# Optimization experiments

Measured on AMD Instinct MI355X. Metric: run time of the kernel, lower is better.

## Reference

```python
import jax, jax.numpy as jnp
import numpy as np

C = 1.0          # curvature
MIN_NORM = 1e-15
EPS = 1e-7       # atanh clamp for fp32

def _sqnorm(x):
    return jnp.sum(x * x, axis=-1, keepdims=True)

def _norm(x):
    return jnp.sqrt(jnp.maximum(_sqnorm(x), MIN_NORM))

def _atanh(u):
    return jnp.arctanh(jnp.clip(u, -1.0 + EPS, 1.0 - EPS))

def mobius_add(x, y, c):
    x2 = _sqnorm(x); y2 = _sqnorm(y)
    xy = jnp.sum(x * y, axis=-1, keepdims=True)
    num = (1.0 + 2.0 * c * xy + c * y2) * x + (1.0 - c * x2) * y
    den = 1.0 + 2.0 * c * xy + c * c * x2 * y2
    return num / jnp.maximum(den, MIN_NORM)

def logmap0(p, c):
    sc = jnp.sqrt(c)
    pn = _norm(p)
    return p / pn / sc * _atanh(sc * pn)

def logmap(p1, p2, c):
    # tangent vector at p1 pointing to p2 (Poincare ball)
    sub = mobius_add(-p1, p2, c)
    sn = _norm(sub)
    lam = 2.0 / jnp.maximum(1.0 - c * _sqnorm(p1), MIN_NORM)
    sc = jnp.sqrt(c)
    return 2.0 / sc / lam * _atanh(sc * sn) * sub / sn

def expmap(p, u, c):
    un = _norm(u)
    lam = 2.0 / jnp.maximum(1.0 - c * _sqnorm(p), MIN_NORM)
    sc = jnp.sqrt(c)
    second = jnp.tanh(sc * lam * un / 2.0) * u / (sc * un)
    return mobius_add(p, second, c)


def setup_inputs() -> dict:
    key = jax.random.key(0)
    k1, k2, k3 = jax.random.split(key, 3)
    B, N, D = 1, 1024, 128
    # points inside the unit Poincare ball (||x|| ~ 0.23)
    x = jax.random.normal(k1, (B, N, D), jnp.float32) * 0.02
    # sparse-ish dense adjacency mask (0/1 floats)
    adj = (jax.random.uniform(k2, (B, N, N)) < 0.05).astype(jnp.float32)
    # DenseAtt: nn.Linear(2*D, 1) weight (flattened) + bias
    att_w = jax.random.normal(k3, (2 * D,), jnp.float32) * 0.1
    att_b = jnp.zeros((), jnp.float32)
    return {"x": x, "adj": adj, "att_w": att_w, "att_b": att_b}


def reference(x, adj, att_w, att_b):
    B, N, D = x.shape
    x_t = logmap0(x, C)                                   # [B,N,D]
    # DenseAtt: sigmoid(Linear(cat(x_i, x_j))) decomposed as left_i + right_j + b
    left = x_t @ att_w[:D]                                # [B,N]
    right = x_t @ att_w[D:]                               # [B,N]
    att = jax.nn.sigmoid(left[:, :, None] + right[:, None, :] + att_b) * adj  # [B,N,N]
    # pairwise logmap: tangent at x_i of every x_j  -> [B,N,N,D]
    x_local = logmap(x[:, :, None, :], x[:, None, :, :], C)
    support_t = jnp.einsum('bij,bijd->bid', att, x_local)  # [B,N,D]
    return expmap(x, support_t, C)
```

## Files before the change

kernel.cpp:

```cpp
#include <hip/hip_runtime.h>
#include <math.h>


typedef short short4v __attribute__((ext_vector_type(4)));
typedef short short8v __attribute__((ext_vector_type(8)));
typedef float float4v __attribute__((ext_vector_type(4)));

static __device__ __forceinline__ short f2bf(float f) {
    unsigned u = __float_as_uint(f);
    u += 0x7fff + ((u >> 16) & 1);
    return (short)(u >> 16);
}
static __device__ __forceinline__ float rcpf(float x) { return __builtin_amdgcn_rcpf(x); }
static __device__ __forceinline__ short8v ld8(const unsigned short* p) {
    short4v lo = *(const short4v*)p;
    short4v hi = *(const short4v*)(p + 4);
    return (short8v){lo[0],lo[1],lo[2],lo[3],hi[0],hi[1],hi[2],hi[3]};
}
static __device__ __forceinline__ float dot4(float4v a, float4v b) {
    return a[0]*b[0] + a[1]*b[1] + a[2]*b[2] + a[3]*b[3];
}
static __device__ __forceinline__ float atanh_over(float pn) {
    float uu = fminf(pn, 1.f - 1e-7f);
    return 0.5f * __logf((1.f + uu) * rcpf(1.f - uu)) * rcpf(pn);
}

__global__ __launch_bounds__(256) void hyp_stats(
    const float* __restrict__ x, const float* __restrict__ w,
    const float* __restrict__ battp,
    float* __restrict__ st_x2, float* __restrict__ st_L, float* __restrict__ st_R)
{
    int row  = blockIdx.x * 4 + (threadIdx.x >> 6);
    int lane = threadIdx.x & 63;
    const float* xr = x + row * 128;
    float a0 = xr[lane], a1 = xr[lane + 64];
    float x2 = a0 * a0 + a1 * a1;
    float dl = a0 * w[lane]       + a1 * w[lane + 64];
    float dr = a0 * w[lane + 128] + a1 * w[lane + 192];
    for (int m = 1; m < 64; m <<= 1) {
        x2 += __shfl_xor(x2, m);
        dl += __shfl_xor(dl, m);
        dr += __shfl_xor(dr, m);
    }
    if (lane == 0) {
        float pn = sqrtf(fmaxf(x2, 1e-15f));
        float f  = atanh_over(pn);
        st_x2[row] = x2;
        st_L[row]  = f * dl + battp[0];
        st_R[row]  = f * dr;
    }
}

__global__ __launch_bounds__(256, 2) void hyp_main(
    const float* __restrict__ x, const float* __restrict__ adj,
    const float* __restrict__ st_x2, const float* __restrict__ st_L,
    const float* __restrict__ st_R,
    float* __restrict__ Yp, float* __restrict__ Sp2)
{
    __shared__ unsigned short sXI [16 * 132];
    __shared__ unsigned short sXJ [128 * 132];
    __shared__ unsigned short sXJt[128 * 132];
    __shared__ unsigned short sW  [16 * 132];

    const int t    = threadIdx.x;
    const int lane = t & 63;
    const int wave = t >> 6;
    const int n    = lane & 15;
    const int q    = lane >> 4;
    const int i0   = blockIdx.x * 16;
    const int c    = blockIdx.y;
    const int j0   = c * 128;

    const float4v* x4 = (const float4v*)x;

    float x2i4[4], bi4[4], li4[4];
#pragma unroll
    for (int r = 0; r < 4; ++r) {
        int i = i0 + q * 4 + r;
        x2i4[r] = st_x2[i];
        li4[r]  = st_L[i];
    }
    float x2j2[2], rj2[2], adjv[2][4];
#pragma unroll
    for (int jsl = 0; jsl < 2; ++jsl) {
        int j = j0 + (wave * 2 + jsl) * 16 + n;
        x2j2[jsl] = st_x2[j];
        rj2[jsl]  = st_R[j];
#pragma unroll
        for (int r = 0; r < 4; ++r)
            adjv[jsl][r] = adj[(i0 + q * 4 + r) * 1024 + j];
    }
#pragma unroll
    for (int r = 0; r < 4; ++r) bi4[r] = 1.f - x2i4[r];

#pragma unroll
    for (int it = 0; it < 2; ++it) {
        int idx = t + it * 256;
        int r = idx >> 5, cc = idx & 31;
        float4v v = x4[(i0 + r) * 32 + cc];
        short4v h = { f2bf(v[0]), f2bf(v[1]), f2bf(v[2]), f2bf(v[3]) };
        *(short4v*)&sXI[r * 132 + cc * 4] = h;
    }
#pragma unroll
    for (int it = 0; it < 4; ++it) {
        int bid = t + it * 256;
        int jr = ((bid >> 4) & 3) | (((bid >> 6) & 7) << 2);
        int dc = (bid & 15) | (((bid >> 9) & 1) << 4);
        float4v v[4];
#pragma unroll
        for (int e = 0; e < 4; ++e)
            v[e] = x4[(j0 + jr * 4 + e) * 32 + dc];
        short4v h[4];
#pragma unroll
        for (int e = 0; e < 4; ++e) {
            h[e] = (short4v){ f2bf(v[e][0]), f2bf(v[e][1]), f2bf(v[e][2]), f2bf(v[e][3]) };
            *(short4v*)&sXJ[(jr * 4 + e) * 132 + dc * 4] = h[e];
        }
#pragma unroll
        for (int d = 0; d < 4; ++d) {
            short4v ht = (short4v){ h[0][d], h[1][d], h[2][d], h[3][d] };
            *(short4v*)&sXJt[(dc * 4 + d) * 132 + jr * 4] = ht;
        }
    }
    __syncthreads();

    short8v afrag[4];
#pragma unroll
    for (int kk = 0; kk < 4; ++kk)
        afrag[kk] = ld8(&sXI[n * 132 + kk * 32 + q * 8]);

    float Sacc[4] = {0.f, 0.f, 0.f, 0.f};

#pragma unroll
    for (int jsl = 0; jsl < 2; ++jsl) {
        int js = wave * 2 + jsl;
        int jrow = js * 16 + n;
        float4v acc = (float4v){0.f, 0.f, 0.f, 0.f};
#pragma unroll
        for (int kk = 0; kk < 4; ++kk) {
            short8v b = ld8(&sXJ[jrow * 132 + kk * 32 + q * 8]);
            acc = __builtin_amdgcn_mfma_f32_16x16x32_bf16(afrag[kk], b, acc, 0, 0, 0);
        }
        float x2j = x2j2[jsl];
        float rj  = rj2[jsl];
#pragma unroll
        for (int r = 0; r < 4; ++r) {
            float G     = acc[r];
            int   i     = q * 4 + r;
            float alpha = 1.f - 2.f * G + x2j;
            float den   = fmaxf(fmaf(x2i4[r], x2j, 1.f - 2.f * G), 1e-15f);
            float rdn   = rcpf(den);
            float bb    = bi4[r];
            float nn2   = alpha * alpha * x2i4[r] + bb * bb * x2j - 2.f * alpha * bb * G;
            float sn    = sqrtf(fmaxf(nn2 * rdn * rdn, 1e-15f));
            float tt    = atanh_over(sn);
            float z     = li4[r] + rj;
            float sig   = rcpf(1.f + __expf(-z));
            float g     = sig * adjv[jsl][r] * tt * rdn;
            Sacc[r]     = fmaf(g, alpha, Sacc[r]);
            sW[i * 132 + js * 16 + n] = (unsigned short)f2bf(g);
        }
    }
    __syncthreads();

    float4v accB[2];
    accB[0] = (float4v){0.f, 0.f, 0.f, 0.f};
    accB[1] = (float4v){0.f, 0.f, 0.f, 0.f};
#pragma unroll
    for (int nsl = 0; nsl < 2; ++nsl) {
        int ns = wave * 2 + nsl;
#pragma unroll
        for (int kk = 0; kk < 4; ++kk) {
            short8v a = ld8(&sW  [n * 132 + kk * 32 + q * 8]);
            short8v b = ld8(&sXJt[(ns * 16 + n) * 132 + kk * 32 + q * 8]);
            accB[nsl] = __builtin_amdgcn_mfma_f32_16x16x32_bf16(a, b, accB[nsl], 0, 0, 0);
        }
    }

    float* Yc = Yp + c * 131072;
#pragma unroll
    for (int nsl = 0; nsl < 2; ++nsl) {
        int ns = wave * 2 + nsl;
#pragma unroll
        for (int r = 0; r < 4; ++r)
            Yc[(i0 + q * 4 + r) * 128 + ns * 16 + n] = accB[nsl][r];
    }
#pragma unroll
    for (int r = 0; r < 4; ++r)
        Sp2[((c * 1024 + i0 + q * 4 + r) * 4 + wave) * 16 + n] = Sacc[r];
}

__global__ __launch_bounds__(256) void hyp_exp(
    const float* __restrict__ x, const float* __restrict__ Yp,
    const float* __restrict__ Sp2, const float* __restrict__ st_x2,
    float* __restrict__ out)
{
    const int t   = threadIdx.x;
    const int row = blockIdx.x * 8 + (t >> 5);
    const int l32 = t & 31;
    float4v y = (float4v){0.f, 0.f, 0.f, 0.f};
    float S = 0.f;
#pragma unroll
    for (int c = 0; c < 8; ++c) {
        y += *(const float4v*)&Yp[c * 131072 + row * 128 + l32 * 4];
        S += Sp2[(c * 1024 + row) * 64 + l32];
        S += Sp2[(c * 1024 + row) * 64 + 32 + l32];
    }
#pragma unroll
    for (int m = 1; m < 32; m <<= 1) S += __shfl_xor(S, m, 32);

    float4v xa = ((const float4v*)x)[row * 32 + l32];
    float x2 = st_x2[row];
    float bE = fmaxf(1.f - x2, 1e-15f);
    float u[4], un2p = 0.f, xup = 0.f;
#pragma unroll
    for (int e = 0; e < 4; ++e) {
        u[e] = bE * (bE * y[e] - S * xa[e]);
        un2p += u[e] * u[e];
        xup  += xa[e] * u[e];
    }
#pragma unroll
    for (int m = 1; m < 32; m <<= 1) {
        un2p += __shfl_xor(un2p, m, 32);
        xup  += __shfl_xor(xup,  m, 32);
    }
    float un  = sqrtf(fmaxf(un2p, 1e-15f));
    float e2  = __expf(2.f * un * rcpf(bE));
    float th  = 1.f - 2.f * rcpf(e2 + 1.f);
    float s2  = th * rcpf(un);
    float xy  = s2 * xup;
    float y2s = th * th;
    float coef = 1.f + 2.f * xy + y2s;
    float den  = fmaxf(1.f + 2.f * xy + x2 * y2s, 1e-15f);
    float rd   = rcpf(den);
    float4v o = { (coef*xa[0] + bE*s2*u[0])*rd, (coef*xa[1] + bE*s2*u[1])*rd,
                  (coef*xa[2] + bE*s2*u[2])*rd, (coef*xa[3] + bE*s2*u[3])*rd };
    ((float4v*)out)[row * 32 + l32] = o;
}

extern "C" void kernel_launch(void* const* d_in, const int* in_sizes, int n_in,
                              void* d_out, int out_size, void* d_ws, size_t ws_size,
                              hipStream_t stream) {
    const float* x    = (const float*)d_in[0];
    const float* adj  = (const float*)d_in[1];
    const float* w    = (const float*)d_in[2];
    const float* batt = (const float*)d_in[3];
    float* out = (float*)d_out;

    float* Yp    = (float*)d_ws;
    float* Sp2   = Yp + 8 * 131072;
    float* st_x2 = Sp2 + 8 * 1024 * 64;
    float* st_L  = st_x2 + 1024;
    float* st_R  = st_L + 1024;

    hipLaunchKernelGGL(hyp_stats, dim3(256), dim3(256), 0, stream,
                       x, w, batt, st_x2, st_L, st_R);
    hipLaunchKernelGGL(hyp_main, dim3(64, 8), dim3(256), 0, stream,
                       x, adj, st_x2, st_L, st_R, Yp, Sp2);
    hipLaunchKernelGGL(hyp_exp, dim3(128), dim3(256), 0, stream,
                       x, Yp, Sp2, st_x2, out);
}
```

Baseline: 72.27 us.

## Precompute swizzled bf16 X and transpose in prep kernel, load via global_load_lds

The stats kernel becomes a prep kernel that also converts x to bf16 in an XOR-swizzled layout and writes a transposed swizzled copy to workspace. The main kernel then fills its LDS tiles with direct global-to-LDS 16-byte loads instead of converting and transposing fp32 data in every block. Shared tiles drop the padding and use XOR swizzling to avoid bank conflicts while allowing 16-byte LDS reads. The trade-off is that the prep kernel runs on only 16 blocks with serial per-thread work, and each block does a full-vmcnt wait before the barrier.

```diff
diff --git a/kernel.cpp b/kernel.cpp
--- a/kernel.cpp
+++ b/kernel.cpp
@@ -11,12 +11,10 @@
     u += 0x7fff + ((u >> 16) & 1);
     return (short)(u >> 16);
 }
+static __device__ __forceinline__ float bf2f(unsigned short s) {
+    return __uint_as_float(((unsigned)s) << 16);
+}
 static __device__ __forceinline__ float rcpf(float x) { return __builtin_amdgcn_rcpf(x); }
-static __device__ __forceinline__ short8v ld8(const unsigned short* p) {
-    short4v lo = *(const short4v*)p;
-    short4v hi = *(const short4v*)(p + 4);
-    return (short8v){lo[0],lo[1],lo[2],lo[3],hi[0],hi[1],hi[2],hi[3]};
-}
 static __device__ __forceinline__ float dot4(float4v a, float4v b) {
     return a[0]*b[0] + a[1]*b[1] + a[2]*b[2] + a[3]*b[3];
 }
@@ -24,43 +22,101 @@
     float uu = fminf(pn, 1.f - 1e-7f);
     return 0.5f * __logf((1.f + uu) * rcpf(1.f - uu)) * rcpf(pn);
 }
-
-__global__ __launch_bounds__(256) void hyp_stats(
+static __device__ __forceinline__ void glds16(const void* g, void* l) {
+    __builtin_amdgcn_global_load_lds(
+        (const __attribute__((address_space(1))) void*)g,
+        (__attribute__((address_space(3))) void*)l, 16, 0, 0);
+}
+
+__global__ __launch_bounds__(256) void hyp_prep(
     const float* __restrict__ x, const float* __restrict__ w,
     const float* __restrict__ battp,
+    unsigned short* __restrict__ XbSw, unsigned short* __restrict__ XbtSw,
     float* __restrict__ st_x2, float* __restrict__ st_L, float* __restrict__ st_R)
 {
-    int row  = blockIdx.x * 4 + (threadIdx.x >> 6);
-    int lane = threadIdx.x & 63;
-    const float* xr = x + row * 128;
-    float a0 = xr[lane], a1 = xr[lane + 64];
-    float x2 = a0 * a0 + a1 * a1;
-    float dl = a0 * w[lane]       + a1 * w[lane + 64];
-    float dr = a0 * w[lane + 128] + a1 * w[lane + 192];
-    for (int m = 1; m < 64; m <<= 1) {
-        x2 += __shfl_xor(x2, m);
-        dl += __shfl_xor(dl, m);
-        dr += __shfl_xor(dr, m);
-    }
-    if (lane == 0) {
-        float pn = sqrtf(fmaxf(x2, 1e-15f));
-        float f  = atanh_over(pn);
-        st_x2[row] = x2;
-        st_L[row]  = f * dl + battp[0];
-        st_R[row]  = f * dr;
+    __shared__ __align__(16) unsigned short sT[128 * 128];
+    __shared__ float sWf[256];
+    __shared__ float sPx[256], sPl[256], sPr[256];
+    const int t  = threadIdx.x;
+    const int bx = blockIdx.x;
+    const bool typeA = bx < 8;
+    const int c  = typeA ? bx : bx - 8;
+    const float4v* x4 = (const float4v*)x;
+    const float4v* w4 = (const float4v*)w;
+
+    if (t < 64) *(float4v*)&sWf[t * 4] = w4[t];
+
+#pragma unroll
+    for (int it = 0; it < 16; ++it) {
+        int idx  = t + it * 256;
+        int r    = idx >> 5;
+        int col4 = idx & 31;
+        float4v v = x4[(c * 128 + r) * 32 + col4];
+        short4v h = { f2bf(v[0]), f2bf(v[1]), f2bf(v[2]), f2bf(v[3]) };
+        int pos = (col4 >> 1) ^ (r & 15);
+        int off = r * 128 + pos * 8 + (col4 & 1) * 4;
+        *(short4v*)&sT[off] = h;
+        if (typeA) *(short4v*)&XbSw[c * 16384 + off] = h;
+    }
+    __syncthreads();
+
+    if (typeA) {
+        int j = t >> 1, ph = t & 1;
+        float x2 = 0.f, dl = 0.f, dr = 0.f;
+#pragma unroll
+        for (int p = 0; p < 8; ++p) {
+            int pp = ph * 8 + p;
+            short8v v = *(const short8v*)&sT[j * 128 + pp * 8];
+            int kbase = (pp ^ (j & 15)) * 8;
+#pragma unroll
+            for (int e = 0; e < 8; ++e) {
+                float f = bf2f((unsigned short)v[e]);
+                x2 = fmaf(f, f, x2);
+                dl = fmaf(f, sWf[kbase + e], dl);
+                dr = fmaf(f, sWf[128 + kbase + e], dr);
+            }
+        }
+        sPx[t] = x2; sPl[t] = dl; sPr[t] = dr;
+        __syncthreads();
+        if (t < 128) {
+            float x2s = sPx[2 * t] + sPx[2 * t + 1];
+            float dls = sPl[2 * t] + sPl[2 * t + 1];
+            float drs = sPr[2 * t] + sPr[2 * t + 1];
+            float pn  = sqrtf(fmaxf(x2s, 1e-15f));
+            float f   = atanh_over(pn);
+            int row = c * 128 + t;
+            st_x2[row] = x2s;
+            st_L [row] = dls * f + battp[0];
+            st_R [row] = drs * f;
+        }
+    } else {
+        int d = t >> 1, jh = t & 1;
+        unsigned short tmp[64];
+#pragma unroll
+        for (int jj = 0; jj < 64; ++jj) {
+            int j = jh * 64 + jj;
+            tmp[jj] = sT[j * 128 + (((d >> 3) ^ (j & 15)) * 8) + (d & 7)];
+        }
+#pragma unroll
+        for (int k8 = 0; k8 < 8; ++k8) {
+            int ktl = jh * 8 + k8;
+            int pt  = ktl ^ (d & 15);
+            *(short8v*)&XbtSw[c * 16384 + d * 128 + pt * 8] = *(const short8v*)&tmp[k8 * 8];
+        }
     }
 }
 
 __global__ __launch_bounds__(256, 2) void hyp_main(
-    const float* __restrict__ x, const float* __restrict__ adj,
+    const unsigned short* __restrict__ XbSw, const unsigned short* __restrict__ XbtSw,
+    const float* __restrict__ adj,
     const float* __restrict__ st_x2, const float* __restrict__ st_L,
     const float* __restrict__ st_R,
     float* __restrict__ Yp, float* __restrict__ Sp2)
 {
-    __shared__ unsigned short sXI [16 * 132];
-    __shared__ unsigned short sXJ [128 * 132];
-    __shared__ unsigned short sXJt[128 * 132];
-    __shared__ unsigned short sW  [16 * 132];
+    __shared__ __align__(16) unsigned short sXI [16 * 128];
+    __shared__ __align__(16) unsigned short sXJ [128 * 128];
+    __shared__ __align__(16) unsigned short sXJt[128 * 128];
+    __shared__ __align__(16) unsigned short sW  [16 * 128];
 
     const int t    = threadIdx.x;
     const int lane = t & 63;
@@ -71,8 +127,6 @@
     const int c    = blockIdx.y;
     const int j0   = c * 128;
 
-    const float4v* x4 = (const float4v*)x;
-
     float x2i4[4], bi4[4], li4[4];
 #pragma unroll
     for (int r = 0; r < 4; ++r) {
@@ -93,43 +147,27 @@
 #pragma unroll
     for (int r = 0; r < 4; ++r) bi4[r] = 1.f - x2i4[r];
 
-#pragma unroll
-    for (int it = 0; it < 2; ++it) {
-        int idx = t + it * 256;
-        int r = idx >> 5, cc = idx & 31;
-        float4v v = x4[(i0 + r) * 32 + cc];
-        short4v h = { f2bf(v[0]), f2bf(v[1]), f2bf(v[2]), f2bf(v[3]) };
-        *(short4v*)&sXI[r * 132 + cc * 4] = h;
-    }
-#pragma unroll
-    for (int it = 0; it < 4; ++it) {
-        int bid = t + it * 256;
-        int jr = ((bid >> 4) & 3) | (((bid >> 6) & 7) << 2);
-        int dc = (bid & 15) | (((bid >> 9) & 1) << 4);
-        float4v v[4];
-#pragma unroll
-        for (int e = 0; e < 4; ++e)
-            v[e] = x4[(j0 + jr * 4 + e) * 32 + dc];
-        short4v h[4];
-#pragma unroll
-        for (int e = 0; e < 4; ++e) {
-            h[e] = (short4v){ f2bf(v[e][0]), f2bf(v[e][1]), f2bf(v[e][2]), f2bf(v[e][3]) };
-            *(short4v*)&sXJ[(jr * 4 + e) * 132 + dc * 4] = h[e];
-        }
-#pragma unroll
-        for (int d = 0; d < 4; ++d) {
-            short4v ht = (short4v){ h[0][d], h[1][d], h[2][d], h[3][d] };
-            *(short4v*)&sXJt[(dc * 4 + d) * 132 + jr * 4] = ht;
-        }
-    }
+    {
+        const char* gXI  = (const char*)(XbSw + i0 * 128);
+        const char* gXJ  = (const char*)(XbSw + c * 16384);
+        const char* gXJt = (const char*)(XbtSw + c * 16384);
+        int wo = wave * 1024 + lane * 16;
+        glds16(gXI + wo, (char*)sXI + wo);
+#pragma unroll
+        for (int it = 0; it < 8; ++it) {
+            glds16(gXJ  + it * 4096 + wo, (char*)sXJ  + it * 4096 + wo);
+            glds16(gXJt + it * 4096 + wo, (char*)sXJt + it * 4096 + wo);
+        }
+    }
+    __builtin_amdgcn_s_waitcnt(0);
     __syncthreads();
 
     short8v afrag[4];
 #pragma unroll
     for (int kk = 0; kk < 4; ++kk)
-        afrag[kk] = ld8(&sXI[n * 132 + kk * 32 + q * 8]);
-
-    float Sacc[4] = {0.f, 0.f, 0.f, 0.f};
+        afrag[kk] = *(const short8v*)&sXI[n * 128 + (((kk * 4 + q) ^ n)) * 8];
+
+    float Sacc[4];
 
 #pragma unroll
     for (int jsl = 0; jsl < 2; ++jsl) {
@@ -138,7 +176,7 @@
         float4v acc = (float4v){0.f, 0.f, 0.f, 0.f};
 #pragma unroll
         for (int kk = 0; kk < 4; ++kk) {
-            short8v b = ld8(&sXJ[jrow * 132 + kk * 32 + q * 8]);
+            short8v b = *(const short8v*)&sXJ[jrow * 128 + (((kk * 4 + q) ^ n)) * 8];
             acc = __builtin_amdgcn_mfma_f32_16x16x32_bf16(afrag[kk], b, acc, 0, 0, 0);
         }
         float x2j = x2j2[jsl];
@@ -157,8 +195,8 @@
             float z     = li4[r] + rj;
             float sig   = rcpf(1.f + __expf(-z));
             float g     = sig * adjv[jsl][r] * tt * rdn;
-            Sacc[r]     = fmaf(g, alpha, Sacc[r]);
-            sW[i * 132 + js * 16 + n] = (unsigned short)f2bf(g);
+            if (jsl == 0) Sacc[r] = g * alpha; else Sacc[r] = fmaf(g, alpha, Sacc[r]);
+            sW[i * 128 + ((js * 2 + (n >> 3)) ^ i) * 8 + (n & 7)] = (unsigned short)f2bf(g);
         }
     }
     __syncthreads();
@@ -169,10 +207,11 @@
 #pragma unroll
     for (int nsl = 0; nsl < 2; ++nsl) {
         int ns = wave * 2 + nsl;
+        int drow = ns * 16 + n;
 #pragma unroll
         for (int kk = 0; kk < 4; ++kk) {
-            short8v a = ld8(&sW  [n * 132 + kk * 32 + q * 8]);
-            short8v b = ld8(&sXJt[(ns * 16 + n) * 132 + kk * 32 + q * 8]);
+            short8v a = *(const short8v*)&sW  [n * 128    + (((kk * 4 + q) ^ n)) * 8];
+            short8v b = *(const short8v*)&sXJt[drow * 128 + (((kk * 4 + q) ^ n)) * 8];
             accB[nsl] = __builtin_amdgcn_mfma_f32_16x16x32_bf16(a, b, accB[nsl], 0, 0, 0);
         }
     }
@@ -252,11 +291,13 @@
     float* st_x2 = Sp2 + 8 * 1024 * 64;
     float* st_L  = st_x2 + 1024;
     float* st_R  = st_L + 1024;
-
-    hipLaunchKernelGGL(hyp_stats, dim3(256), dim3(256), 0, stream,
-                       x, w, batt, st_x2, st_L, st_R);
+    unsigned short* XbSw  = (unsigned short*)(st_R + 1024);
+    unsigned short* XbtSw = XbSw + 131072;
+
+    hipLaunchKernelGGL(hyp_prep, dim3(16), dim3(256), 0, stream,
+                       x, w, batt, XbSw, XbtSw, st_x2, st_L, st_R);
     hipLaunchKernelGGL(hyp_main, dim3(64, 8), dim3(256), 0, stream,
-                       x, adj, st_x2, st_L, st_R, Yp, Sp2);
+                       XbSw, XbtSw, adj, st_x2, st_L, st_R, Yp, Sp2);
     hipLaunchKernelGGL(hyp_exp, dim3(128), dim3(256), 0, stream,
                        x, Yp, Sp2, st_x2, out);
 }
```

After: 79.11 us. 9.5% more time.
